# Kernel optimization log

Hardware: AMD Instinct MI355X
Metric: run time of the kernel (lower is better)

Reference implementation:

```python
import jax, jax.numpy as jnp
import numpy as np

N_GROUP = 8
TOPK_GROUP = 4
TOP_K = 8
ROUTED_SCALING = 2.5
NUM_EXPERTS = 256
HIDDEN = 7168
TOKENS = 8192


def setup_inputs() -> dict:
    key = jax.random.key(0)
    k1, k2, k3 = jax.random.split(key, 3)
    hidden_states = jax.random.normal(k1, (TOKENS, HIDDEN), dtype=jnp.float32)
    weight = jax.random.normal(k2, (NUM_EXPERTS, HIDDEN), dtype=jnp.float32) * 0.02
    e_score_correction_bias = jax.random.normal(k3, (NUM_EXPERTS,), dtype=jnp.float32) * 0.1
    return {"hidden_states": hidden_states, "weight": weight,
            "e_score_correction_bias": e_score_correction_bias}


def reference(hidden_states, weight, e_score_correction_bias):
    # logits = x @ W^T  (fp32 gate GEMM)
    logits = jnp.einsum('th,eh->te', hidden_states.astype(jnp.float32), weight)
    scores = jax.nn.sigmoid(logits)                       # [T, E]
    swb = scores + e_score_correction_bias                # [T, E]
    T, E = swb.shape
    gsize = E // N_GROUP
    # per-group score = sum of top-2 biased scores within each group
    grouped = swb.reshape(T, N_GROUP, gsize)
    top2, _ = jax.lax.top_k(grouped, 2)                   # [T, G, 2]
    group_scores = top2.sum(axis=-1)                      # [T, G]
    # keep topk_group groups
    _, gidx = jax.lax.top_k(group_scores, TOPK_GROUP)     # [T, topk_group]
    rows = jnp.arange(T)[:, None]
    group_mask = jnp.zeros((T, N_GROUP), jnp.float32).at[rows, gidx].set(1.0)
    score_mask = jnp.repeat(group_mask, gsize, axis=-1)   # [T, E]
    swb_masked = swb * score_mask
    # top_k experts among kept groups
    _, tidx = jax.lax.top_k(swb_masked, TOP_K)            # [T, top_k]
    new_mask = jnp.zeros((T, E), jnp.float32).at[rows, tidx].set(1.0)
    sel = scores * new_mask
    score_sum = sel.sum(axis=-1, keepdims=True) + 1e-20
    return sel / score_sum * ROUTED_SCALING
```

## Files before the change

### kernel.cpp

```cpp
#include <hip/hip_runtime.h>
#include <math.h>

#define TOKENS   8192
#define HIDDEN   7168
#define NEXPERT  256
#define NGROUP   8
#define TOPKG    4
#define TOPK     8
#define SCALE    2.5f

#define BM 128
#define BN 128
#define BK 32
#define KSPLIT 4
#define KPB (HIDDEN / KSPLIT)
#define NT  (KPB / BK)
#define TILE_BYTES 16384

#define RSTR 72

typedef _Float16 half8 __attribute__((ext_vector_type(8)));
typedef _Float16 half4 __attribute__((ext_vector_type(4)));
typedef float    floatx4 __attribute__((ext_vector_type(4)));

__device__ __forceinline__ void cvt_store(_Float16* __restrict__ H,
                                          int row, int k0, float4 v) {
    half4 h, l;
    h[0] = (_Float16)v.x; h[1] = (_Float16)v.y;
    h[2] = (_Float16)v.z; h[3] = (_Float16)v.w;
    l[0] = (_Float16)(v.x - (float)h[0]);
    l[1] = (_Float16)(v.y - (float)h[1]);
    l[2] = (_Float16)(v.z - (float)h[2]);
    l[3] = (_Float16)(v.w - (float)h[3]);
    const int base = row * RSTR + ((k0 >> 3) << 4) + (k0 & 7);
    *(half4*)&H[base]     = h;
    *(half4*)&H[base + 8] = l;
}

__device__ __forceinline__ void cvt8(const float4 a, const float4 b,
                                     half8& h, half8& l) {
    h[0] = (_Float16)a.x; h[1] = (_Float16)a.y;
    h[2] = (_Float16)a.z; h[3] = (_Float16)a.w;
    h[4] = (_Float16)b.x; h[5] = (_Float16)b.y;
    h[6] = (_Float16)b.z; h[7] = (_Float16)b.w;
    l[0] = (_Float16)(a.x - (float)h[0]); l[1] = (_Float16)(a.y - (float)h[1]);
    l[2] = (_Float16)(a.z - (float)h[2]); l[3] = (_Float16)(a.w - (float)h[3]);
    l[4] = (_Float16)(b.x - (float)h[4]); l[5] = (_Float16)(b.y - (float)h[5]);
    l[6] = (_Float16)(b.z - (float)h[6]); l[7] = (_Float16)(b.w - (float)h[7]);
}

__global__ __launch_bounds__(256) void zero_kernel(float* __restrict__ O) {
    const int i = blockIdx.x * 256 + threadIdx.x;
    *(float4*)&O[(size_t)i * 4] = float4{0.f, 0.f, 0.f, 0.f};
}

__global__ __launch_bounds__(896) void wsplit_kernel(
    const float* __restrict__ W, char* __restrict__ WS)
{
    const int e  = blockIdx.x;
    const int og = threadIdx.x;
    const float4 a = *(const float4*)&W[(size_t)e * HIDDEN + og * 8];
    const float4 b = *(const float4*)&W[(size_t)e * HIDDEN + og * 8 + 4];
    half8 h, l;
    cvt8(a, b, h, l);

    const int kz  = og / 224;
    const int tt  = (og % 224) >> 2;
    const int oc  = og & 3;
    const int row = e & 127, nb = e >> 7;
    char* p = WS + (size_t)((nb * KSPLIT + kz) * NT + tt) * TILE_BYTES
            + (row * 4 + oc) * 32;
    *(half8*)p        = h;
    *(half8*)(p + 16) = l;
}

__global__ __launch_bounds__(256, 2) void gate_gemm_kernel(
    const float* __restrict__ X, const char* __restrict__ WS,
    float* __restrict__ OUT)
{
    __shared__ _Float16 Ab[2][BM * RSTR];
    __shared__ _Float16 Bb[2][BN * RSTR];

    const int tid = threadIdx.x;
    const int nb  = blockIdx.x * BN;
    const int mb  = blockIdx.y * BM;
    const int kb  = blockIdx.z * KPB;

    const int srow = tid >> 3;
    const int sk0  = (tid & 7) * 4;
    const float* Aptr = X + (size_t)(mb + srow) * HIDDEN + kb + sk0;

    const char* Wimg =
        WS + (size_t)((blockIdx.x * KSPLIT + blockIdx.z) * NT) * TILE_BYTES;
    const int brow[2] = { tid >> 2, (tid + 256) >> 2 };
    const int boct    = tid & 3;
    const int bbase[2] = { brow[0] * RSTR + boct * 16,
                           brow[1] * RSTR + boct * 16 };

    float4 av[4];
    half8  nh[2], nl[2];
#pragma unroll
    for (int q = 0; q < 4; q++)
        av[q] = *(const float4*)(Aptr + (size_t)(q * 32) * HIDDEN);
#pragma unroll
    for (int s = 0; s < 2; s++) {
        const char* src = Wimg + (tid + 256 * s) * 32;
        nh[s] = *(const half8*)src;
        nl[s] = *(const half8*)(src + 16);
    }
#pragma unroll
    for (int q = 0; q < 4; q++)
        cvt_store(Ab[0], q * 32 + srow, sk0, av[q]);
#pragma unroll
    for (int s = 0; s < 2; s++) {
        *(half8*)&Bb[0][bbase[s]]     = nh[s];
        *(half8*)&Bb[0][bbase[s] + 8] = nl[s];
    }

    const int lane = tid & 63, wave = tid >> 6;
    const int wm = (wave >> 1) * 64, wn = (wave & 1) * 64;
    const int fr = lane & 15, quad = lane >> 4;

    floatx4 acc[4][4];
#pragma unroll
    for (int i = 0; i < 4; i++)
#pragma unroll
        for (int j = 0; j < 4; j++) acc[i][j] = floatx4{0.f, 0.f, 0.f, 0.f};

    for (int t = 0; t < NT; t++) {
        if (t + 1 < NT) {
            const int o = (t + 1) * BK;
#pragma unroll
            for (int q = 0; q < 4; q++)
                av[q] = *(const float4*)(Aptr + o + (size_t)(q * 32) * HIDDEN);
            const char* srcT = Wimg + (size_t)(t + 1) * TILE_BYTES;
#pragma unroll
            for (int s = 0; s < 2; s++) {
                const char* src = srcT + (tid + 256 * s) * 32;
                nh[s] = *(const half8*)src;
                nl[s] = *(const half8*)(src + 16);
            }
        }

        __syncthreads();

        const _Float16* __restrict__ Ac = Ab[t & 1];
        const _Float16* __restrict__ Bc = Bb[t & 1];

        half8 ah[4], al[4];
#pragma unroll
        for (int i = 0; i < 4; i++) {
            const int a = (wm + i * 16 + fr) * RSTR + quad * 16;
            ah[i] = *(const half8*)&Ac[a];
            al[i] = *(const half8*)&Ac[a + 8];
        }
#pragma unroll
        for (int j = 0; j < 4; j++) {
            const int b = (wn + j * 16 + fr) * RSTR + quad * 16;
            const half8 bh = *(const half8*)&Bc[b];
            const half8 bl = *(const half8*)&Bc[b + 8];
#pragma unroll
            for (int i = 0; i < 4; i++) {
                acc[i][j] = __builtin_amdgcn_mfma_f32_16x16x32_f16(
                    al[i], bh, acc[i][j], 0, 0, 0);
                acc[i][j] = __builtin_amdgcn_mfma_f32_16x16x32_f16(
                    ah[i], bl, acc[i][j], 0, 0, 0);
                acc[i][j] = __builtin_amdgcn_mfma_f32_16x16x32_f16(
                    ah[i], bh, acc[i][j], 0, 0, 0);
            }
        }

        if (t + 1 < NT) {
            _Float16* An = Ab[(t + 1) & 1];
            _Float16* Bn = Bb[(t + 1) & 1];
#pragma unroll
            for (int q = 0; q < 4; q++)
                cvt_store(An, q * 32 + srow, sk0, av[q]);
#pragma unroll
            for (int s = 0; s < 2; s++) {
                *(half8*)&Bn[bbase[s]]     = nh[s];
                *(half8*)&Bn[bbase[s] + 8] = nl[s];
            }
        }
    }

#pragma unroll
    for (int i = 0; i < 4; i++)
#pragma unroll
        for (int j = 0; j < 4; j++) {
            const int col = nb + wn + j * 16 + fr;
#pragma unroll
            for (int r = 0; r < 4; r++) {
                const int row = mb + wm + i * 16 + quad * 4 + r;
                atomicAdd(&OUT[(size_t)row * NEXPERT + col], acc[i][j][r]);
            }
        }
}

__global__ __launch_bounds__(256) void route_kernel(
    float* __restrict__ S, const float* __restrict__ bias)
{
    const int lane = threadIdx.x & 63;
    const int wave = threadIdx.x >> 6;
    const int t    = blockIdx.x * 4 + wave;

    const float4 lg4 = *(const float4*)&S[(size_t)t * NEXPERT + lane * 4];
    const float4 b4  = *(const float4*)&bias[lane * 4];
    float sc[4];
    sc[0] = 1.0f / (1.0f + expf(-lg4.x));
    sc[1] = 1.0f / (1.0f + expf(-lg4.y));
    sc[2] = 1.0f / (1.0f + expf(-lg4.z));
    sc[3] = 1.0f / (1.0f + expf(-lg4.w));
    float swb[4] = { sc[0] + b4.x, sc[1] + b4.y, sc[2] + b4.z, sc[3] + b4.w };

    float m1 = -INFINITY, m2 = -INFINITY;
#pragma unroll
    for (int j = 0; j < 4; j++) {
        const float v = swb[j];
        if (v > m1)      { m2 = m1; m1 = v; }
        else if (v > m2) { m2 = v; }
    }
#pragma unroll
    for (int s = 1; s < 8; s <<= 1) {
        const float o1 = __shfl_xor(m1, s, 64);
        const float o2 = __shfl_xor(m2, s, 64);
        const float hi = fmaxf(m1, o1);
        const float lo = fminf(m1, o1);
        m2 = fmaxf(lo, fmaxf(m2, o2));
        m1 = hi;
    }
    const float gs = m1 + m2;

    float gsc[NGROUP];
#pragma unroll
    for (int g = 0; g < NGROUP; g++) gsc[g] = __shfl(gs, g * 8, 64);
    const int myg = lane >> 3;
    int rank = 0;
#pragma unroll
    for (int g = 0; g < NGROUP; g++)
        rank += (gsc[g] > gs) || (gsc[g] == gs && g < myg);
    const bool kept = (rank < TOPKG);

    float v[4];
#pragma unroll
    for (int j = 0; j < 4; j++) v[j] = kept ? swb[j] : 0.0f;

    float sum = 0.0f;
    int selmask = 0;
    for (int r = 0; r < TOPK; r++) {
        float bv = -INFINITY;
        int   bi = 0x7fffffff;
#pragma unroll
        for (int j = 0; j < 4; j++) {
            const bool avail = ((selmask >> j) & 1) == 0;
            if (avail && v[j] > bv) { bv = v[j]; bi = lane * 4 + j; }
        }
#pragma unroll
        for (int s = 1; s < 64; s <<= 1) {
            const float ov = __shfl_xor(bv, s, 64);
            const int   oi = __shfl_xor(bi, s, 64);
            if (ov > bv || (ov == bv && oi < bi)) { bv = ov; bi = oi; }
        }
        const int wl = bi >> 2, wj = bi & 3;
        const float mysc = (wj == 0) ? sc[0] : (wj == 1) ? sc[1]
                         : (wj == 2) ? sc[2] : sc[3];
        sum += __shfl(mysc, wl, 64);
        if (lane == wl) selmask |= (1 << wj);
    }

    const float rcp = SCALE / (sum + 1e-20f);
    float4 o;
    o.x = (selmask & 1) ? sc[0] * rcp : 0.0f;
    o.y = (selmask & 2) ? sc[1] * rcp : 0.0f;
    o.z = (selmask & 4) ? sc[2] * rcp : 0.0f;
    o.w = (selmask & 8) ? sc[3] * rcp : 0.0f;
    *(float4*)&S[(size_t)t * NEXPERT + lane * 4] = o;
}

extern "C" void kernel_launch(void* const* d_in, const int* in_sizes, int n_in,
                              void* d_out, int out_size, void* d_ws, size_t ws_size,
                              hipStream_t stream) {
    const float* X    = (const float*)d_in[0];
    const float* W    = (const float*)d_in[1];
    const float* bias = (const float*)d_in[2];
    float* out = (float*)d_out;
    char* ws = (char*)d_ws; (void)ws_size;

    zero_kernel<<<(TOKENS * NEXPERT / 4) / 256, 256, 0, stream>>>(out);
    wsplit_kernel<<<NEXPERT, 896, 0, stream>>>(W, ws);
    dim3 ggrid(NEXPERT / BN, TOKENS / BM, KSPLIT);
    gate_gemm_kernel<<<ggrid, 256, 0, stream>>>(X, ws, out);
    route_kernel<<<TOKENS / 4, 256, 0, stream>>>(out, bias);
}
```

Measured before the change: 385.2 us.

## Widen GEMM tile to all experts, use 32x32 MFMA with interleaved clusters

The gate GEMM now uses a 128x256 tile covering all 256 experts, so each block converts X to split-fp16 once instead of twice. It runs 8 waves per block and switches to 32x32x16 MFMA instructions. The loop is split into four MFMA clusters separated by barriers, with s_setprio raised around them, and the next tile's LDS stores are interleaved between clusters. The goal is to remove redundant X loads and conversions and to improve MFMA density. The cost is many more barriers per iteration, a halved grid (256 blocks), larger LDS use and more register pressure.

```diff
diff --git a/kernel.cpp b/kernel.cpp
--- a/kernel.cpp
+++ b/kernel.cpp
@@ -10,32 +10,17 @@
 #define SCALE    2.5f
 
 #define BM 128
-#define BN 128
+#define BN 256
 #define BK 32
 #define KSPLIT 4
 #define KPB (HIDDEN / KSPLIT)
 #define NT  (KPB / BK)
-#define TILE_BYTES 16384
+#define WTILE_BYTES 32768
 
 #define RSTR 72
 
-typedef _Float16 half8 __attribute__((ext_vector_type(8)));
-typedef _Float16 half4 __attribute__((ext_vector_type(4)));
-typedef float    floatx4 __attribute__((ext_vector_type(4)));
-
-__device__ __forceinline__ void cvt_store(_Float16* __restrict__ H,
-                                          int row, int k0, float4 v) {
-    half4 h, l;
-    h[0] = (_Float16)v.x; h[1] = (_Float16)v.y;
-    h[2] = (_Float16)v.z; h[3] = (_Float16)v.w;
-    l[0] = (_Float16)(v.x - (float)h[0]);
-    l[1] = (_Float16)(v.y - (float)h[1]);
-    l[2] = (_Float16)(v.z - (float)h[2]);
-    l[3] = (_Float16)(v.w - (float)h[3]);
-    const int base = row * RSTR + ((k0 >> 3) << 4) + (k0 & 7);
-    *(half4*)&H[base]     = h;
-    *(half4*)&H[base + 8] = l;
-}
+typedef _Float16 half8   __attribute__((ext_vector_type(8)));
+typedef float    floatx16 __attribute__((ext_vector_type(16)));
 
 __device__ __forceinline__ void cvt8(const float4 a, const float4 b,
                                      half8& h, half8& l) {
@@ -64,17 +49,15 @@
     half8 h, l;
     cvt8(a, b, h, l);
 
-    const int kz  = og / 224;
-    const int tt  = (og % 224) >> 2;
-    const int oc  = og & 3;
-    const int row = e & 127, nb = e >> 7;
-    char* p = WS + (size_t)((nb * KSPLIT + kz) * NT + tt) * TILE_BYTES
-            + (row * 4 + oc) * 32;
+    const int kz = og / 224;
+    const int tt = (og % 224) >> 2;
+    const int oc = og & 3;
+    char* p = WS + (size_t)(kz * NT + tt) * WTILE_BYTES + (e * 4 + oc) * 32;
     *(half8*)p        = h;
     *(half8*)(p + 16) = l;
 }
 
-__global__ __launch_bounds__(256, 2) void gate_gemm_kernel(
+__global__ __launch_bounds__(512, 2) void gate_gemm_kernel(
     const float* __restrict__ X, const char* __restrict__ WS,
     float* __restrict__ OUT)
 {
@@ -82,117 +65,145 @@
     __shared__ _Float16 Bb[2][BN * RSTR];
 
     const int tid = threadIdx.x;
-    const int nb  = blockIdx.x * BN;
-    const int mb  = blockIdx.y * BM;
-    const int kb  = blockIdx.z * KPB;
-
-    const int srow = tid >> 3;
-    const int sk0  = (tid & 7) * 4;
-    const float* Aptr = X + (size_t)(mb + srow) * HIDDEN + kb + sk0;
-
-    const char* Wimg =
-        WS + (size_t)((blockIdx.x * KSPLIT + blockIdx.z) * NT) * TILE_BYTES;
-    const int brow[2] = { tid >> 2, (tid + 256) >> 2 };
-    const int boct    = tid & 3;
-    const int bbase[2] = { brow[0] * RSTR + boct * 16,
-                           brow[1] * RSTR + boct * 16 };
-
-    float4 av[4];
-    half8  nh[2], nl[2];
-#pragma unroll
-    for (int q = 0; q < 4; q++)
-        av[q] = *(const float4*)(Aptr + (size_t)(q * 32) * HIDDEN);
-#pragma unroll
-    for (int s = 0; s < 2; s++) {
-        const char* src = Wimg + (tid + 256 * s) * 32;
-        nh[s] = *(const half8*)src;
-        nl[s] = *(const half8*)(src + 16);
-    }
-#pragma unroll
-    for (int q = 0; q < 4; q++)
-        cvt_store(Ab[0], q * 32 + srow, sk0, av[q]);
-#pragma unroll
-    for (int s = 0; s < 2; s++) {
-        *(half8*)&Bb[0][bbase[s]]     = nh[s];
-        *(half8*)&Bb[0][bbase[s] + 8] = nl[s];
-    }
+    const int mb  = blockIdx.x * BM;
+    const int kb  = blockIdx.y * KPB;
+
+    const int arow = tid >> 2, aoct = tid & 3;
+    const float* Aptr = X + (size_t)(mb + arow) * HIDDEN + kb + aoct * 8;
+    const int alb = arow * RSTR + aoct * 16;
+
+    const char* Wimg = WS + (size_t)blockIdx.y * NT * WTILE_BYTES;
+    const int boff0 = tid * 32;
+    const int boff1 = (tid + 512) * 32;
+    const int blb0  = (tid >> 2) * RSTR + (tid & 3) * 16;
+    const int blb1  = ((tid >> 2) + 128) * RSTR + (tid & 3) * 16;
 
     const int lane = tid & 63, wave = tid >> 6;
-    const int wm = (wave >> 1) * 64, wn = (wave & 1) * 64;
-    const int fr = lane & 15, quad = lane >> 4;
-
-    floatx4 acc[4][4];
-#pragma unroll
-    for (int i = 0; i < 4; i++)
-#pragma unroll
-        for (int j = 0; j < 4; j++) acc[i][j] = floatx4{0.f, 0.f, 0.f, 0.f};
-
-    for (int t = 0; t < NT; t++) {
-        if (t + 1 < NT) {
-            const int o = (t + 1) * BK;
-#pragma unroll
-            for (int q = 0; q < 4; q++)
-                av[q] = *(const float4*)(Aptr + o + (size_t)(q * 32) * HIDDEN);
-            const char* srcT = Wimg + (size_t)(t + 1) * TILE_BYTES;
-#pragma unroll
-            for (int s = 0; s < 2; s++) {
-                const char* src = srcT + (tid + 256 * s) * 32;
-                nh[s] = *(const half8*)src;
-                nl[s] = *(const half8*)(src + 16);
-            }
-        }
-
-        __syncthreads();
-
-        const _Float16* __restrict__ Ac = Ab[t & 1];
-        const _Float16* __restrict__ Bc = Bb[t & 1];
-
-        half8 ah[4], al[4];
-#pragma unroll
-        for (int i = 0; i < 4; i++) {
-            const int a = (wm + i * 16 + fr) * RSTR + quad * 16;
-            ah[i] = *(const half8*)&Ac[a];
-            al[i] = *(const half8*)&Ac[a + 8];
-        }
-#pragma unroll
-        for (int j = 0; j < 4; j++) {
-            const int b = (wn + j * 16 + fr) * RSTR + quad * 16;
-            const half8 bh = *(const half8*)&Bc[b];
-            const half8 bl = *(const half8*)&Bc[b + 8];
-#pragma unroll
-            for (int i = 0; i < 4; i++) {
-                acc[i][j] = __builtin_amdgcn_mfma_f32_16x16x32_f16(
-                    al[i], bh, acc[i][j], 0, 0, 0);
-                acc[i][j] = __builtin_amdgcn_mfma_f32_16x16x32_f16(
-                    ah[i], bl, acc[i][j], 0, 0, 0);
-                acc[i][j] = __builtin_amdgcn_mfma_f32_16x16x32_f16(
-                    ah[i], bh, acc[i][j], 0, 0, 0);
-            }
-        }
-
-        if (t + 1 < NT) {
-            _Float16* An = Ab[(t + 1) & 1];
-            _Float16* Bn = Bb[(t + 1) & 1];
-#pragma unroll
-            for (int q = 0; q < 4; q++)
-                cvt_store(An, q * 32 + srow, sk0, av[q]);
-#pragma unroll
-            for (int s = 0; s < 2; s++) {
-                *(half8*)&Bn[bbase[s]]     = nh[s];
-                *(half8*)&Bn[bbase[s] + 8] = nl[s];
-            }
-        }
-    }
-
-#pragma unroll
-    for (int i = 0; i < 4; i++)
-#pragma unroll
-        for (int j = 0; j < 4; j++) {
-            const int col = nb + wn + j * 16 + fr;
-#pragma unroll
-            for (int r = 0; r < 4; r++) {
-                const int row = mb + wm + i * 16 + quad * 4 + r;
-                atomicAdd(&OUT[(size_t)row * NEXPERT + col], acc[i][j][r]);
+    const int wm  = (wave >> 2) * 64;
+    const int wn  = (wave & 3) * 64;
+    const int r32 = lane & 31;
+    const int kb16 = (lane >> 5) * 16;
+
+    {
+        const half8 h0 = *(const half8*)(Wimg + boff0);
+        const half8 l0 = *(const half8*)(Wimg + boff0 + 16);
+        const half8 h1 = *(const half8*)(Wimg + boff1);
+        const half8 l1 = *(const half8*)(Wimg + boff1 + 16);
+        const float4 a0 = *(const float4*)Aptr;
+        const float4 a1 = *(const float4*)(Aptr + 4);
+        *(half8*)&Bb[0][blb0]     = h0;
+        *(half8*)&Bb[0][blb0 + 8] = l0;
+        *(half8*)&Bb[0][blb1]     = h1;
+        *(half8*)&Bb[0][blb1 + 8] = l1;
+        half8 ha, la;
+        cvt8(a0, a1, ha, la);
+        *(half8*)&Ab[0][alb]     = ha;
+        *(half8*)&Ab[0][alb + 8] = la;
+    }
+    __syncthreads();
+
+    floatx16 acc[2][2];
+#pragma unroll
+    for (int i = 0; i < 2; i++)
+#pragma unroll
+        for (int j = 0; j < 2; j++)
+#pragma unroll
+            for (int r = 0; r < 16; r++) acc[i][j][r] = 0.f;
+
+#define MFMA_CLUSTER(i, j)                                                    \
+    __builtin_amdgcn_s_setprio(1);                                            \
+    _Pragma("unroll")                                                         \
+    for (int s = 0; s < 2; s++) {                                             \
+        acc[i][j] = __builtin_amdgcn_mfma_f32_32x32x16_f16(                   \
+            aL[i][s], bH[j][s], acc[i][j], 0, 0, 0);                          \
+        acc[i][j] = __builtin_amdgcn_mfma_f32_32x32x16_f16(                   \
+            aH[i][s], bL[j][s], acc[i][j], 0, 0, 0);                          \
+        acc[i][j] = __builtin_amdgcn_mfma_f32_32x32x16_f16(                   \
+            aH[i][s], bH[j][s], acc[i][j], 0, 0, 0);                          \
+    }                                                                         \
+    __builtin_amdgcn_s_setprio(0);
+
+    for (int t = 0; t < NT; ++t) {
+        const _Float16* Ac = Ab[t & 1];
+        const _Float16* Bc = Bb[t & 1];
+        _Float16* An = Ab[(t + 1) & 1];
+        _Float16* Bn = Bb[(t + 1) & 1];
+        const bool pre = (t + 1 < NT);
+
+        half8 aH[2][2], aL[2][2], bH[2][2], bL[2][2];
+
+        half8 nb0h, nb0l, nb1h, nb1l; float4 na0, na1;
+        if (pre) {
+            const char* wsrc = Wimg + (size_t)(t + 1) * WTILE_BYTES;
+            nb0h = *(const half8*)(wsrc + boff0);
+            nb0l = *(const half8*)(wsrc + boff0 + 16);
+            nb1h = *(const half8*)(wsrc + boff1);
+            nb1l = *(const half8*)(wsrc + boff1 + 16);
+            const float* asrc = Aptr + (t + 1) * BK;
+            na0 = *(const float4*)asrc;
+            na1 = *(const float4*)(asrc + 4);
+        }
+#pragma unroll
+        for (int s = 0; s < 2; s++) {
+            const int ao = (wm + r32) * RSTR + s * 32 + kb16;
+            aH[0][s] = *(const half8*)&Ac[ao];
+            aL[0][s] = *(const half8*)&Ac[ao + 8];
+            const int bo = (wn + r32) * RSTR + s * 32 + kb16;
+            bH[0][s] = *(const half8*)&Bc[bo];
+            bL[0][s] = *(const half8*)&Bc[bo + 8];
+        }
+        __syncthreads();
+        MFMA_CLUSTER(0, 0)
+        __syncthreads();
+
+#pragma unroll
+        for (int s = 0; s < 2; s++) {
+            const int bo = (wn + 32 + r32) * RSTR + s * 32 + kb16;
+            bH[1][s] = *(const half8*)&Bc[bo];
+            bL[1][s] = *(const half8*)&Bc[bo + 8];
+        }
+        __syncthreads();
+        MFMA_CLUSTER(0, 1)
+        __syncthreads();
+
+#pragma unroll
+        for (int s = 0; s < 2; s++) {
+            const int ao = (wm + 32 + r32) * RSTR + s * 32 + kb16;
+            aH[1][s] = *(const half8*)&Ac[ao];
+            aL[1][s] = *(const half8*)&Ac[ao + 8];
+        }
+        if (pre) {
+            *(half8*)&Bn[blb0]     = nb0h;
+            *(half8*)&Bn[blb0 + 8] = nb0l;
+            *(half8*)&Bn[blb1]     = nb1h;
+            *(half8*)&Bn[blb1 + 8] = nb1l;
+        }
+        __syncthreads();
+        MFMA_CLUSTER(1, 0)
+        __syncthreads();
+
+        if (pre) {
+            half8 ha, la;
+            cvt8(na0, na1, ha, la);
+            *(half8*)&An[alb]     = ha;
+            *(half8*)&An[alb + 8] = la;
+        }
+        __syncthreads();
+        MFMA_CLUSTER(1, 1)
+        __syncthreads();
+    }
+#undef MFMA_CLUSTER
+
+#pragma unroll
+    for (int i = 0; i < 2; i++)
+#pragma unroll
+        for (int j = 0; j < 2; j++) {
+            const int col = wn + j * 32 + r32;
+#pragma unroll
+            for (int reg = 0; reg < 16; reg++) {
+                const int row = mb + wm + i * 32
+                              + (reg & 3) + 8 * (reg >> 2) + 4 * (lane >> 5);
+                atomicAdd(&OUT[(size_t)row * NEXPERT + col], acc[i][j][reg]);
             }
         }
 }
@@ -288,7 +299,7 @@
 
     zero_kernel<<<(TOKENS * NEXPERT / 4) / 256, 256, 0, stream>>>(out);
     wsplit_kernel<<<NEXPERT, 896, 0, stream>>>(W, ws);
-    dim3 ggrid(NEXPERT / BN, TOKENS / BM, KSPLIT);
-    gate_gemm_kernel<<<ggrid, 256, 0, stream>>>(X, ws, out);
+    dim3 ggrid(TOKENS / BM, KSPLIT);
+    gate_gemm_kernel<<<ggrid, 512, 0, stream>>>(X, ws, out);
     route_kernel<<<TOKENS / 4, 256, 0, stream>>>(out, bias);
 }
```

After: 419.6 us. 8.9% more time.

## Single-buffer LDS, double split-K, raise occupancy, fuse zeroing into weight split

Applied to the files above, without the earlier changes.

Replaces the double-buffered LDS tiles with a single buffer synchronized twice per iteration, halving shared memory so four blocks per CU can be resident. Split-K goes from 4 to 8 to create more blocks and give the scheduler more waves to hide latency. The output-zeroing kernel is folded into the weight-split kernel, removing one launch. In exchange each iteration carries an extra barrier, there is less intra-block overlap, register pressure is tighter, and atomic adds to the output double.

```diff
diff --git a/kernel.cpp b/kernel.cpp
--- a/kernel.cpp
+++ b/kernel.cpp
@@ -12,7 +12,7 @@
 #define BM 128
 #define BN 128
 #define BK 32
-#define KSPLIT 4
+#define KSPLIT 8
 #define KPB (HIDDEN / KSPLIT)
 #define NT  (KPB / BK)
 #define TILE_BYTES 16384
@@ -49,14 +49,17 @@
     l[6] = (_Float16)(b.z - (float)h[6]); l[7] = (_Float16)(b.w - (float)h[7]);
 }
 
-__global__ __launch_bounds__(256) void zero_kernel(float* __restrict__ O) {
-    const int i = blockIdx.x * 256 + threadIdx.x;
-    *(float4*)&O[(size_t)i * 4] = float4{0.f, 0.f, 0.f, 0.f};
-}
-
 __global__ __launch_bounds__(896) void wsplit_kernel(
-    const float* __restrict__ W, char* __restrict__ WS)
+    const float* __restrict__ W, char* __restrict__ WS, float* __restrict__ O)
 {
+    const int gt = blockIdx.x * 896 + threadIdx.x;
+#pragma unroll
+    for (int i = 0; i < 3; i++) {
+        const int idx = gt + i * (NEXPERT * 896);
+        if (idx < TOKENS * NEXPERT / 4)
+            *(float4*)&O[(size_t)idx * 4] = float4{0.f, 0.f, 0.f, 0.f};
+    }
+
     const int e  = blockIdx.x;
     const int og = threadIdx.x;
     const float4 a = *(const float4*)&W[(size_t)e * HIDDEN + og * 8];
@@ -64,9 +67,9 @@
     half8 h, l;
     cvt8(a, b, h, l);
 
-    const int kz  = og / 224;
-    const int tt  = (og % 224) >> 2;
-    const int oc  = og & 3;
+    const int kz = og / (KPB / 8);
+    const int tt = (og % (KPB / 8)) >> 2;
+    const int oc = og & 3;
     const int row = e & 127, nb = e >> 7;
     char* p = WS + (size_t)((nb * KSPLIT + kz) * NT + tt) * TILE_BYTES
             + (row * 4 + oc) * 32;
@@ -74,12 +77,12 @@
     *(half8*)(p + 16) = l;
 }
 
-__global__ __launch_bounds__(256, 2) void gate_gemm_kernel(
+__global__ __launch_bounds__(256, 4) void gate_gemm_kernel(
     const float* __restrict__ X, const char* __restrict__ WS,
     float* __restrict__ OUT)
 {
-    __shared__ _Float16 Ab[2][BM * RSTR];
-    __shared__ _Float16 Bb[2][BN * RSTR];
+    __shared__ _Float16 Ab[BM * RSTR];
+    __shared__ _Float16 Bb[BN * RSTR];
 
     const int tid = threadIdx.x;
     const int nb  = blockIdx.x * BN;
@@ -92,10 +95,8 @@
 
     const char* Wimg =
         WS + (size_t)((blockIdx.x * KSPLIT + blockIdx.z) * NT) * TILE_BYTES;
-    const int brow[2] = { tid >> 2, (tid + 256) >> 2 };
-    const int boct    = tid & 3;
-    const int bbase[2] = { brow[0] * RSTR + boct * 16,
-                           brow[1] * RSTR + boct * 16 };
+    const int bbase[2] = { (tid >> 2) * RSTR + (tid & 3) * 16,
+                           ((tid >> 2) + 64) * RSTR + (tid & 3) * 16 };
 
     float4 av[4];
     half8  nh[2], nl[2];
@@ -108,14 +109,6 @@
         nh[s] = *(const half8*)src;
         nl[s] = *(const half8*)(src + 16);
     }
-#pragma unroll
-    for (int q = 0; q < 4; q++)
-        cvt_store(Ab[0], q * 32 + srow, sk0, av[q]);
-#pragma unroll
-    for (int s = 0; s < 2; s++) {
-        *(half8*)&Bb[0][bbase[s]]     = nh[s];
-        *(half8*)&Bb[0][bbase[s] + 8] = nl[s];
-    }
 
     const int lane = tid & 63, wave = tid >> 6;
     const int wm = (wave >> 1) * 64, wn = (wave & 1) * 64;
@@ -128,6 +121,17 @@
         for (int j = 0; j < 4; j++) acc[i][j] = floatx4{0.f, 0.f, 0.f, 0.f};
 
     for (int t = 0; t < NT; t++) {
+#pragma unroll
+        for (int q = 0; q < 4; q++)
+            cvt_store(Ab, q * 32 + srow, sk0, av[q]);
+#pragma unroll
+        for (int s = 0; s < 2; s++) {
+            *(half8*)&Bb[bbase[s]]     = nh[s];
+            *(half8*)&Bb[bbase[s] + 8] = nl[s];
+        }
+
+        __syncthreads();
+
         if (t + 1 < NT) {
             const int o = (t + 1) * BK;
 #pragma unroll
@@ -142,23 +146,18 @@
             }
         }
 
-        __syncthreads();
-
-        const _Float16* __restrict__ Ac = Ab[t & 1];
-        const _Float16* __restrict__ Bc = Bb[t & 1];
-
         half8 ah[4], al[4];
 #pragma unroll
         for (int i = 0; i < 4; i++) {
             const int a = (wm + i * 16 + fr) * RSTR + quad * 16;
-            ah[i] = *(const half8*)&Ac[a];
-            al[i] = *(const half8*)&Ac[a + 8];
+            ah[i] = *(const half8*)&Ab[a];
+            al[i] = *(const half8*)&Ab[a + 8];
         }
 #pragma unroll
         for (int j = 0; j < 4; j++) {
             const int b = (wn + j * 16 + fr) * RSTR + quad * 16;
-            const half8 bh = *(const half8*)&Bc[b];
-            const half8 bl = *(const half8*)&Bc[b + 8];
+            const half8 bh = *(const half8*)&Bb[b];
+            const half8 bl = *(const half8*)&Bb[b + 8];
 #pragma unroll
             for (int i = 0; i < 4; i++) {
                 acc[i][j] = __builtin_amdgcn_mfma_f32_16x16x32_f16(
@@ -170,18 +169,7 @@
             }
         }
 
-        if (t + 1 < NT) {
-            _Float16* An = Ab[(t + 1) & 1];
-            _Float16* Bn = Bb[(t + 1) & 1];
-#pragma unroll
-            for (int q = 0; q < 4; q++)
-                cvt_store(An, q * 32 + srow, sk0, av[q]);
-#pragma unroll
-            for (int s = 0; s < 2; s++) {
-                *(half8*)&Bn[bbase[s]]     = nh[s];
-                *(half8*)&Bn[bbase[s] + 8] = nl[s];
-            }
-        }
+        __syncthreads();
     }
 
 #pragma unroll
@@ -286,8 +274,7 @@
     float* out = (float*)d_out;
     char* ws = (char*)d_ws; (void)ws_size;
 
-    zero_kernel<<<(TOKENS * NEXPERT / 4) / 256, 256, 0, stream>>>(out);
-    wsplit_kernel<<<NEXPERT, 896, 0, stream>>>(W, ws);
+    wsplit_kernel<<<NEXPERT, 896, 0, stream>>>(W, ws, out);
     dim3 ggrid(NEXPERT / BN, TOKENS / BM, KSPLIT);
     gate_gemm_kernel<<<ggrid, 256, 0, stream>>>(X, ws, out);
     route_kernel<<<TOKENS / 4, 256, 0, stream>>>(out, bias);
```

After: 401.9 us. +4.4%, slower.
